# Kernel optimization log

Measured on AMD Instinct MI355X. Metric: run time of the kernel, lower is better.

Reference implementation:

```python
import math
import jax, jax.numpy as jnp
import numpy as np

B, T, C = 2, 2048, 2048
H, G = 16, 4
D = C // H  # head_dim = 128
KV = G * D
SOFT_CAP = 50.0
EPS = 1e-6


def setup_inputs() -> dict:
    key = jax.random.key(0)
    ks = jax.random.split(key, 5)
    s = 1.0 / math.sqrt(C)
    return {
        "x": jax.random.normal(ks[0], (B, T, C), jnp.float32),
        "Wq": jax.random.normal(ks[1], (C, C), jnp.float32) * s,
        "Wk": jax.random.normal(ks[2], (KV, C), jnp.float32) * s,
        "Wv": jax.random.normal(ks[3], (KV, C), jnp.float32) * s,
        "Wo": jax.random.normal(ks[4], (C, C), jnp.float32) * s,
        "bo": jnp.zeros((C,), jnp.float32),
        "q_norm_w": jnp.ones((D,), jnp.float32),
        "k_norm_w": jnp.ones((D,), jnp.float32),
    }


def _rmsnorm(x, w):
    # norm/sqrt(d) formulation, eps added to rms (matches torch module exactly)
    rms = jnp.linalg.norm(x, axis=-1, keepdims=True) / math.sqrt(x.shape[-1])
    return w * (x / (rms + EPS))


def _rotary_tables(seq_len, dim):
    inv_freq = 1.0 / (10000.0 ** (jnp.arange(0, dim, 2, dtype=jnp.float32) / dim))
    t = jnp.arange(seq_len, dtype=jnp.float32)
    freqs = jnp.outer(t, inv_freq)  # [T, D/2]
    return jnp.cos(freqs), jnp.sin(freqs)


def _apply_rope(x, cos, sin):
    # x: [B, T, h, D]; cos/sin: [T, D/2] broadcast as [1, T, 1, D/2]
    d = x.shape[-1] // 2
    x1, x2 = x[..., :d], x[..., d:]
    c = cos[None, :, None, :]
    s = sin[None, :, None, :]
    return jnp.concatenate([x1 * c + x2 * s, -x1 * s + x2 * c], axis=-1)


def reference(x, Wq, Wk, Wv, Wo, bo, q_norm_w, k_norm_w):
    b, t, c = x.shape
    q = (x @ Wq.T).reshape(b, t, H, D)
    k = (x @ Wk.T).reshape(b, t, G, D)
    v = (x @ Wv.T).reshape(b, t, G, D)

    cos, sin = _rotary_tables(t, D)
    q = _apply_rope(_rmsnorm(q, q_norm_w), cos, sin)
    k = _apply_rope(_rmsnorm(k, k_norm_w), cos, sin)

    q = q.transpose(0, 2, 1, 3)              # [B, H, T, D]
    k = jnp.repeat(k.transpose(0, 2, 1, 3), H // G, axis=1)  # [B, H, T, D]
    v = jnp.repeat(v.transpose(0, 2, 1, 3), H // G, axis=1)

    att = jnp.einsum("bhqd,bhkd->bhqk", q, k) / math.sqrt(D)
    causal = jnp.tril(jnp.ones((t, t), bool))
    att = jnp.where(causal[None, None], att, -jnp.inf)
    att = SOFT_CAP * jnp.tanh(att / SOFT_CAP)  # masked entries -> -50
    att = jax.nn.softmax(att, axis=-1)

    y = jnp.einsum("bhqk,bhkd->bhqd", att, v)
    y = y.transpose(0, 2, 1, 3).reshape(b, t, c)
    return y @ Wo.T + bo
```

## Files before the change

kernel.cpp:

```cpp
#include <hip/hip_runtime.h>
#include <math.h>

#define T_SEQ 2048
#define C_DIM 2048
#define NH    16
#define NG    4
#define DH    128
#define BATCH 2

typedef unsigned short u16;
typedef __bf16 bf16_t;
typedef bf16_t bf16x8 __attribute__((ext_vector_type(8)));
typedef float  f32x4  __attribute__((ext_vector_type(4)));

static __device__ __forceinline__ u16 f2bf(float f) {
    return __builtin_bit_cast(u16, (__bf16)f);
}

static __device__ __forceinline__ void gll16(const void* g, void* lds) {
    __builtin_amdgcn_global_load_lds(
        (const __attribute__((address_space(1))) void*)(unsigned long long)(g),
        (__attribute__((address_space(3))) void*)(unsigned int)(unsigned long long)(lds),
        16, 0, 0);
}

__global__ __launch_bounds__(256)
void cast_multi(const float* __restrict__ x,  const float* __restrict__ wq,
                const float* __restrict__ wk, const float* __restrict__ wv,
                u16* __restrict__ xo, u16* __restrict__ wqo,
                u16* __restrict__ wko, u16* __restrict__ wvo) {
    int i = blockIdx.x * 256 + threadIdx.x;
    const float* src; u16* dst; int off;
    if (i < 1048576)      { src = x;  dst = xo;  off = i; }
    else if (i < 1572864) { src = wq; dst = wqo; off = i - 1048576; }
    else if (i < 1703936) { src = wk; dst = wko; off = i - 1572864; }
    else                  { src = wv; dst = wvo; off = i - 1703936; }
    const float4* p = (const float4*)src + (size_t)off * 2;
    float4 a = p[0], b = p[1];
    u16 u[8] = {f2bf(a.x), f2bf(a.y), f2bf(a.z), f2bf(a.w),
                f2bf(b.x), f2bf(b.y), f2bf(b.z), f2bf(b.w)};
    *(uint4*)(dst + (size_t)off * 8) = *(const uint4*)u;
}

__global__ __launch_bounds__(256)
void cast_f32_bf16(const float* __restrict__ in, u16* __restrict__ out, int n8) {
    int i = blockIdx.x * 256 + threadIdx.x;
    if (i >= n8) return;
    const float4* p = (const float4*)in + (size_t)i * 2;
    float4 a = p[0], b = p[1];
    u16 u[8] = {f2bf(a.x), f2bf(a.y), f2bf(a.z), f2bf(a.w),
                f2bf(b.x), f2bf(b.y), f2bf(b.z), f2bf(b.w)};
    *(uint4*)(out + (size_t)i * 8) = *(const uint4*)u;
}

static __device__ __forceinline__ void gemm_body(
        u16* As, u16* Bs,
        const u16* __restrict__ A, const u16* __restrict__ B,
        const float* __restrict__ bias, float* __restrict__ C,
        int N, int K, int m0, int n0) {
    const int t    = threadIdx.x;
    const int lane = t & 63, w = t >> 6;
    const int l15  = lane & 15, quad = lane >> 4;
    const int wr   = w >> 1, wc = w & 1;

    f32x4 acc[4][4];
#pragma unroll
    for (int mt = 0; mt < 4; ++mt)
#pragma unroll
        for (int nt = 0; nt < 4; ++nt) acc[mt][nt] = (f32x4){0.f, 0.f, 0.f, 0.f};

    const int off0 = w*2048 + lane*16;
    const int r0 = off0 >> 6,          c0 = (off0 & 63) >> 1;
    const int r1 = (off0+1024) >> 6,   c1 = ((off0+1024) & 63) >> 1;
    const u16* Ag0 = A + (size_t)(m0 + r0) * K + c0;
    const u16* Ag1 = A + (size_t)(m0 + r1) * K + c1;
    const u16* Bg0 = B + (size_t)(n0 + r0) * K + c0;
    const u16* Bg1 = B + (size_t)(n0 + r1) * K + c1;
    char* AsB = (char*)As; char* BsB = (char*)Bs;
    const int ldsOff0 = w*2048, ldsOff1 = w*2048 + 1024;

    for (int k0 = 0; k0 < K; k0 += 32) {
        gll16(Ag0 + k0, AsB + ldsOff0);
        gll16(Ag1 + k0, AsB + ldsOff1);
        gll16(Bg0 + k0, BsB + ldsOff0);
        gll16(Bg1 + k0, BsB + ldsOff1);
        __syncthreads();
        bf16x8 af[4], bf[4];
#pragma unroll
        for (int mt = 0; mt < 4; ++mt)
            af[mt] = __builtin_bit_cast(bf16x8,
                *(const uint4*)&As[(wr*64 + mt*16 + l15)*32 + quad*8]);
#pragma unroll
        for (int nt = 0; nt < 4; ++nt)
            bf[nt] = __builtin_bit_cast(bf16x8,
                *(const uint4*)&Bs[(wc*64 + nt*16 + l15)*32 + quad*8]);
#pragma unroll
        for (int mt = 0; mt < 4; ++mt)
#pragma unroll
            for (int nt = 0; nt < 4; ++nt)
                acc[mt][nt] = __builtin_amdgcn_mfma_f32_16x16x32_bf16(
                                  af[mt], bf[nt], acc[mt][nt], 0, 0, 0);
        __syncthreads();
    }

#pragma unroll
    for (int mt = 0; mt < 4; ++mt)
#pragma unroll
        for (int nt = 0; nt < 4; ++nt) {
            const int col = n0 + wc*64 + nt*16 + l15;
            const float bv = bias ? bias[col] : 0.f;
#pragma unroll
            for (int r = 0; r < 4; ++r) {
                const int row = m0 + wr*64 + mt*16 + quad*4 + r;
                C[(size_t)row * N + col] = acc[mt][nt][r] + bv;
            }
        }
}

__global__ __launch_bounds__(256)
void gemm_nt_bf16(const u16* __restrict__ A, const u16* __restrict__ B,
                  const float* __restrict__ bias, float* __restrict__ C,
                  int N, int K) {
    __shared__ __align__(16) u16 As[128*32];
    __shared__ __align__(16) u16 Bs[128*32];
    gemm_body(As, Bs, A, B, bias, C, N, K, blockIdx.y*128, blockIdx.x*128);
}

__global__ __launch_bounds__(256)
void gemm_qkv(const u16* __restrict__ A,  const u16* __restrict__ Bq,
              const u16* __restrict__ Bk, const u16* __restrict__ Bv,
              float* __restrict__ Cq, float* __restrict__ Ck, float* __restrict__ Cv) {
    __shared__ __align__(16) u16 As[128*32];
    __shared__ __align__(16) u16 Bs[128*32];
    const int bx = blockIdx.x;
    const u16* B; float* C; int N, n0;
    if (bx < 16)      { B = Bq; C = Cq; N = 2048; n0 = bx * 128; }
    else if (bx < 20) { B = Bk; C = Ck; N = 512;  n0 = (bx-16) * 128; }
    else              { B = Bv; C = Cv; N = 512;  n0 = (bx-20) * 128; }
    gemm_body(As, Bs, A, B, nullptr, C, N, 2048, blockIdx.y*128, n0);
}

__global__ __launch_bounds__(256)
void rmsnorm_rope_qk(const float* __restrict__ qf, const float* __restrict__ kf,
                     const float* __restrict__ qw, const float* __restrict__ kw,
                     u16* __restrict__ qo, u16* __restrict__ ko) {
    const int blk  = blockIdx.x;
    const int sub  = threadIdx.x >> 6;
    const int lane = threadIdx.x & 63;
    const float* in; const float* w; u16* out; int row, nheads; float scale;
    if (blk < 16384) {
        in = qf; w = qw; out = qo; nheads = NH; scale = 0.08838834764831845f;
        row = blk * 4 + sub;
    } else {
        in = kf; w = kw; out = ko; nheads = NG; scale = 1.0f;
        row = (blk - 16384) * 4 + sub;
    }
    const float* p = in + (size_t)row * 128;
    float x1 = p[lane], x2 = p[lane + 64];
    float ss = x1*x1 + x2*x2;
#pragma unroll
    for (int off = 32; off >= 1; off >>= 1) ss += __shfl_xor(ss, off, 64);
    float inv = 1.0f / (sqrtf(ss * (1.0f/128.0f)) + 1e-6f);
    float x1n = w[lane]      * x1 * inv;
    float x2n = w[lane + 64] * x2 * inv;
    int tpos = (row / nheads) & (T_SEQ - 1);
    float invfreq = powf(10000.0f, -(float)lane / 64.0f);
    float s, c;
    sincosf((float)tpos * invfreq, &s, &c);
    out[(size_t)row*128 + lane]      = f2bf((x1n * c + x2n * s) * scale);
    out[(size_t)row*128 + lane + 64] = f2bf((x2n * c - x1n * s) * scale);
}

__global__ __launch_bounds__(256)
void v_cast_transpose(const float* __restrict__ v, u16* __restrict__ vt) {
    __shared__ u16 Lt[128 * 66];
    const int t  = threadIdx.x;
    const int t0 = blockIdx.x * 64;
    const int bg = blockIdx.y;
    const int b  = bg / NG, g = bg % NG;
#pragma unroll
    for (int rep = 0; rep < 8; ++rep) {
        int idx = rep * 256 + t;
        int i   = idx >> 5;
        int c   = idx & 31;
        float4 f = *(const float4*)(v + ((size_t)(b*T_SEQ + t0 + i)*NG + g)*DH + c*4);
        Lt[(c*4+0)*66 + i] = f2bf(f.x);
        Lt[(c*4+1)*66 + i] = f2bf(f.y);
        Lt[(c*4+2)*66 + i] = f2bf(f.z);
        Lt[(c*4+3)*66 + i] = f2bf(f.w);
    }
    __syncthreads();
#pragma unroll
    for (int rep = 0; rep < 4; ++rep) {
        int idx = rep * 256 + t;
        int d = idx >> 3, c = idx & 7;
        const u16* src = &Lt[d*66 + c*8];
        uint4 val;
        val.x = *(const unsigned int*)(src + 0);
        val.y = *(const unsigned int*)(src + 2);
        val.z = *(const unsigned int*)(src + 4);
        val.w = *(const unsigned int*)(src + 6);
        *(uint4*)(vt + ((size_t)(bg*DH + d))*T_SEQ + t0 + c*8) = val;
    }
}

#define KPAD 136
#define VPAD 72
#define PPAD 72

__global__ __launch_bounds__(512)
void flash_attn_mfma(const u16* __restrict__ qh, const u16* __restrict__ kh,
                     const u16* __restrict__ vt, u16* __restrict__ y) {
    __shared__ __align__(16) u16 Ks [64  * KPAD];
    __shared__ __align__(16) u16 Vts[128 * VPAD];
    __shared__ __align__(16) u16 Ps [128 * PPAD];

    const int t    = threadIdx.x;
    const int lane = t & 63, w = t >> 6;
    const int l15  = lane & 15, quad = lane >> 4;
    const int bg   = blockIdx.y;
    const int b    = bg >> 2, g = bg & 3;
    const int chunk = b ? (int)blockIdx.x : (63 - (int)blockIdx.x);
    const int q0   = chunk * 32;
    const int h    = g * (NH / NG) + (w & 3);
    const int qrow0 = q0 + (w >> 2) * 16;

    const float L2E = 1.4426950408889634f;

    bf16x8 aq[4];
    const u16* qp = qh + ((size_t)(b*T_SEQ + qrow0 + l15) * NH + h) * DH;
#pragma unroll
    for (int kc = 0; kc < 4; ++kc)
        aq[kc] = __builtin_bit_cast(bf16x8, *(const uint4*)(qp + kc*32 + quad*8));

    f32x4 accO[8];
#pragma unroll
    for (int nd = 0; nd < 8; ++nd) accO[nd] = (f32x4){0.f, 0.f, 0.f, 0.f};
    float ls[4] = {0.f, 0.f, 0.f, 0.f};

    const int kr = t >> 4, kc16 = t & 15;
    const int vd = t >> 3, vc8  = t & 7;
    const u16* kgb = kh + ((size_t)b*T_SEQ*NG + g)*DH;
    const u16* vgb = vt + ((size_t)(b*NG + g)*DH)*T_SEQ;

    uint4 kreg0, kreg1, vreg0, vreg1;
    {
        kreg0 = *(const uint4*)(kgb + (size_t)(0 + kr)      * NG*DH + kc16*8);
        kreg1 = *(const uint4*)(kgb + (size_t)(0 + kr + 32) * NG*DH + kc16*8);
        vreg0 = *(const uint4*)(vgb + (size_t)vd       * T_SEQ + 0 + vc8*8);
        vreg1 = *(const uint4*)(vgb + (size_t)(vd + 64)* T_SEQ + 0 + vc8*8);
    }

    const int ktiles = q0 / 64 + 1;
    for (int kt = 0; kt < ktiles; ++kt) {
        *(uint4*)&Ks [ kr      *KPAD + kc16*8] = kreg0;
        *(uint4*)&Ks [(kr + 32)*KPAD + kc16*8] = kreg1;
        *(uint4*)&Vts[ vd      *VPAD + vc8*8]  = vreg0;
        *(uint4*)&Vts[(vd + 64)*VPAD + vc8*8]  = vreg1;
        __syncthreads();

        if (kt + 1 < ktiles) {
            const int k1 = (kt + 1) * 64;
            kreg0 = *(const uint4*)(kgb + (size_t)(k1 + kr)      * NG*DH + kc16*8);
            kreg1 = *(const uint4*)(kgb + (size_t)(k1 + kr + 32) * NG*DH + kc16*8);
            vreg0 = *(const uint4*)(vgb + (size_t)vd       * T_SEQ + k1 + vc8*8);
            vreg1 = *(const uint4*)(vgb + (size_t)(vd + 64)* T_SEQ + k1 + vc8*8);
        }

        const int k0 = kt * 64;
        f32x4 accS[4];
#pragma unroll
        for (int nt = 0; nt < 4; ++nt) accS[nt] = (f32x4){0.f, 0.f, 0.f, 0.f};
#pragma unroll
        for (int nt = 0; nt < 4; ++nt)
#pragma unroll
            for (int kc = 0; kc < 4; ++kc) {
                bf16x8 bk = __builtin_bit_cast(bf16x8,
                    *(const uint4*)&Ks[(nt*16 + l15)*KPAD + kc*32 + quad*8]);
                accS[nt] = __builtin_amdgcn_mfma_f32_16x16x32_bf16(aq[kc], bk, accS[nt], 0, 0, 0);
            }

#pragma unroll
        for (int nt = 0; nt < 4; ++nt) {
            const int colg = k0 + nt*16 + l15;
#pragma unroll
            for (int r = 0; r < 4; ++r) {
                const int rowg = qrow0 + quad*4 + r;
                float s = accS[nt][r];
                float z = s * 0.02f;
                float u = z * z;
                float poly = fmaf(u, fmaf(u, fmaf(u, -0.05396825396825397f,
                                       0.13333333333333333f),
                                      -0.3333333333333333f), 1.0f);
                float p = __builtin_amdgcn_exp2f(s * poly * L2E);
                p = (colg > rowg) ? 0.f : p;
                ls[r] += p;
                Ps[(w*16 + quad*4 + r)*PPAD + nt*16 + l15] = f2bf(p);
            }
        }

        bf16x8 ap[2];
#pragma unroll
        for (int kc = 0; kc < 2; ++kc)
            ap[kc] = __builtin_bit_cast(bf16x8,
                *(const uint4*)&Ps[(w*16 + l15)*PPAD + kc*32 + quad*8]);

#pragma unroll
        for (int nd = 0; nd < 8; ++nd)
#pragma unroll
            for (int kc = 0; kc < 2; ++kc) {
                bf16x8 bv = __builtin_bit_cast(bf16x8,
                    *(const uint4*)&Vts[(nd*16 + l15)*VPAD + kc*32 + quad*8]);
                accO[nd] = __builtin_amdgcn_mfma_f32_16x16x32_bf16(ap[kc], bv, accO[nd], 0, 0, 0);
            }
        __syncthreads();
    }

#pragma unroll
    for (int r = 0; r < 4; ++r) {
        float v = ls[r];
        v += __shfl_xor(v, 1, 64);
        v += __shfl_xor(v, 2, 64);
        v += __shfl_xor(v, 4, 64);
        v += __shfl_xor(v, 8, 64);
        ls[r] = v;
    }

#pragma unroll
    for (int r = 0; r < 4; ++r) {
        float invl = 1.f / ls[r];
        u16* yp = y + (size_t)(b*T_SEQ + qrow0 + quad*4 + r) * C_DIM + h*DH;
#pragma unroll
        for (int nd = 0; nd < 8; ++nd)
            yp[nd*16 + l15] = f2bf(accO[nd][r] * invl);
    }
}

extern "C" void kernel_launch(void* const* d_in, const int* in_sizes, int n_in,
                              void* d_out, int out_size, void* d_ws, size_t ws_size,
                              hipStream_t stream) {
    const float* x  = (const float*)d_in[0];
    const float* Wq = (const float*)d_in[1];
    const float* Wk = (const float*)d_in[2];
    const float* Wv = (const float*)d_in[3];
    const float* Wo = (const float*)d_in[4];
    const float* bo = (const float*)d_in[5];
    const float* qw = (const float*)d_in[6];
    const float* kw = (const float*)d_in[7];
    float* out = (float*)d_out;

    const size_t qE = (size_t)BATCH * T_SEQ * NH * DH;
    const size_t kE = (size_t)BATCH * T_SEQ * NG * DH;
    const size_t wqE = (size_t)C_DIM * C_DIM;

    float* qf  = (float*)d_ws;
    float* kf  = qf + qE;
    float* vf  = kf + kE;
    u16*   qh  = (u16*)(vf + kE);
    u16*   khb = qh + qE;
    u16*   vtb = khb + kE;
    u16*   xh  = vtb + kE;
    u16*   wqh = xh + qE;
    u16*   wkh = wqh + wqE;
    u16*   wvh = wkh + (size_t)(NG*DH)*C_DIM;
    u16*   woh = (u16*)kf;
    u16*   yh  = (u16*)qf;

    const int M = BATCH * T_SEQ;
    dim3 blk(256);

    cast_multi<<<dim3(7168), blk, 0, stream>>>(x, Wq, Wk, Wv, xh, wqh, wkh, wvh);

    gemm_qkv<<<dim3(24, M/128), blk, 0, stream>>>(xh, wqh, wkh, wvh, qf, kf, vf);

    rmsnorm_rope_qk<<<dim3(M*NH/4 + M*NG/4), blk, 0, stream>>>(qf, kf, qw, kw, qh, khb);
    v_cast_transpose<<<dim3(T_SEQ/64, BATCH*NG), blk, 0, stream>>>(vf, vtb);

    cast_f32_bf16<<<dim3(wqE/8/256), blk, 0, stream>>>(Wo, woh, wqE/8);

    flash_attn_mfma<<<dim3(T_SEQ/32, BATCH*NG), dim3(512), 0, stream>>>(qh, khb, vtb, yh);

    gemm_nt_bf16<<<dim3(C_DIM/128, M/128), blk, 0, stream>>>(yh, woh, bo, out, C_DIM, C_DIM);
}
```

Measured before the change: 386.7 us.

## Double-buffer K/V via direct-to-LDS loads with swizzle, two query tiles per wave

The flash attention kernel now runs 256 threads. Each wave owns one head and handles two 16-row query tiles, so every K/V fragment read from LDS feeds two MFMAs. K and V tiles are loaded straight into double-buffered LDS with global_load_lds. XOR swizzling replaces row padding to avoid bank conflicts, which removes the register staging and the trailing barrier per tile. The trade-off is more accumulator registers per wave and half as many waves per block, which could reduce latency hiding.

```diff
diff --git a/kernel.cpp b/kernel.cpp
--- a/kernel.cpp
+++ b/kernel.cpp
@@ -204,16 +204,12 @@
     }
 }
 
-#define KPAD 136
-#define VPAD 72
-#define PPAD 72
-
-__global__ __launch_bounds__(512)
+__global__ __launch_bounds__(256, 2)
 void flash_attn_mfma(const u16* __restrict__ qh, const u16* __restrict__ kh,
                      const u16* __restrict__ vt, u16* __restrict__ y) {
-    __shared__ __align__(16) u16 Ks [64  * KPAD];
-    __shared__ __align__(16) u16 Vts[128 * VPAD];
-    __shared__ __align__(16) u16 Ps [128 * PPAD];
+    __shared__ __align__(16) u16 Ks[2][64*128];
+    __shared__ __align__(16) u16 Vs[2][128*64];
+    __shared__ __align__(16) u16 Ps[64*64];
 
     const int t    = threadIdx.x;
     const int lane = t & 63, w = t >> 6;
@@ -222,118 +218,143 @@
     const int b    = bg >> 2, g = bg & 3;
     const int chunk = b ? (int)blockIdx.x : (63 - (int)blockIdx.x);
     const int q0   = chunk * 32;
-    const int h    = g * (NH / NG) + (w & 3);
-    const int qrow0 = q0 + (w >> 2) * 16;
+    const int h    = g * (NH / NG) + w;
 
     const float L2E = 1.4426950408889634f;
 
-    bf16x8 aq[4];
-    const u16* qp = qh + ((size_t)(b*T_SEQ + qrow0 + l15) * NH + h) * DH;
-#pragma unroll
-    for (int kc = 0; kc < 4; ++kc)
-        aq[kc] = __builtin_bit_cast(bf16x8, *(const uint4*)(qp + kc*32 + quad*8));
-
-    f32x4 accO[8];
-#pragma unroll
-    for (int nd = 0; nd < 8; ++nd) accO[nd] = (f32x4){0.f, 0.f, 0.f, 0.f};
-    float ls[4] = {0.f, 0.f, 0.f, 0.f};
-
-    const int kr = t >> 4, kc16 = t & 15;
-    const int vd = t >> 3, vc8  = t & 7;
+    bf16x8 aq[2][4];
+#pragma unroll
+    for (int m = 0; m < 2; ++m) {
+        const u16* qp = qh + ((size_t)(b*T_SEQ + q0 + m*16 + l15) * NH + h) * DH;
+#pragma unroll
+        for (int kc = 0; kc < 4; ++kc)
+            aq[m][kc] = __builtin_bit_cast(bf16x8, *(const uint4*)(qp + kc*32 + quad*8));
+    }
+
+    f32x4 accO[2][8];
+#pragma unroll
+    for (int m = 0; m < 2; ++m)
+#pragma unroll
+        for (int nd = 0; nd < 8; ++nd) accO[m][nd] = (f32x4){0.f, 0.f, 0.f, 0.f};
+    float ls[2][4] = {{0.f,0.f,0.f,0.f},{0.f,0.f,0.f,0.f}};
+
     const u16* kgb = kh + ((size_t)b*T_SEQ*NG + g)*DH;
     const u16* vgb = vt + ((size_t)(b*NG + g)*DH)*T_SEQ;
 
-    uint4 kreg0, kreg1, vreg0, vreg1;
-    {
-        kreg0 = *(const uint4*)(kgb + (size_t)(0 + kr)      * NG*DH + kc16*8);
-        kreg1 = *(const uint4*)(kgb + (size_t)(0 + kr + 32) * NG*DH + kc16*8);
-        vreg0 = *(const uint4*)(vgb + (size_t)vd       * T_SEQ + 0 + vc8*8);
-        vreg1 = *(const uint4*)(vgb + (size_t)(vd + 64)* T_SEQ + 0 + vc8*8);
-    }
-
-    const int ktiles = q0 / 64 + 1;
+    const int krb = t >> 4, kcl = t & 15;
+    const int vdb = t >> 3, vcl = t & 7;
+
+    const int ktiles = q0/64 + 1;
+
+#pragma unroll
+    for (int j = 0; j < 4; ++j) {
+        const int kr = j*16 + krb;
+        gll16(kgb + (size_t)kr*(NG*DH) + ((kcl ^ (kr & 7)) << 3),
+              (char*)Ks[0] + j*4096 + w*1024);
+        const int vd = j*32 + vdb;
+        gll16(vgb + (size_t)vd*T_SEQ + ((vcl ^ (vd & 7)) << 3),
+              (char*)Vs[0] + j*4096 + w*1024);
+    }
+
     for (int kt = 0; kt < ktiles; ++kt) {
-        *(uint4*)&Ks [ kr      *KPAD + kc16*8] = kreg0;
-        *(uint4*)&Ks [(kr + 32)*KPAD + kc16*8] = kreg1;
-        *(uint4*)&Vts[ vd      *VPAD + vc8*8]  = vreg0;
-        *(uint4*)&Vts[(vd + 64)*VPAD + vc8*8]  = vreg1;
+        asm volatile("s_waitcnt vmcnt(0)" ::: "memory");
         __syncthreads();
 
         if (kt + 1 < ktiles) {
-            const int k1 = (kt + 1) * 64;
-            kreg0 = *(const uint4*)(kgb + (size_t)(k1 + kr)      * NG*DH + kc16*8);
-            kreg1 = *(const uint4*)(kgb + (size_t)(k1 + kr + 32) * NG*DH + kc16*8);
-            vreg0 = *(const uint4*)(vgb + (size_t)vd       * T_SEQ + k1 + vc8*8);
-            vreg1 = *(const uint4*)(vgb + (size_t)(vd + 64)* T_SEQ + k1 + vc8*8);
-        }
-
+            const int k0n = (kt + 1) * 64, bn = (kt + 1) & 1;
+#pragma unroll
+            for (int j = 0; j < 4; ++j) {
+                const int kr = j*16 + krb;
+                gll16(kgb + (size_t)(k0n + kr)*(NG*DH) + ((kcl ^ (kr & 7)) << 3),
+                      (char*)Ks[bn] + j*4096 + w*1024);
+                const int vd = j*32 + vdb;
+                gll16(vgb + (size_t)vd*T_SEQ + k0n + ((vcl ^ (vd & 7)) << 3),
+                      (char*)Vs[bn] + j*4096 + w*1024);
+            }
+        }
+
+        const u16* Kb = Ks[kt & 1];
+        const u16* Vb = Vs[kt & 1];
         const int k0 = kt * 64;
-        f32x4 accS[4];
-#pragma unroll
-        for (int nt = 0; nt < 4; ++nt) accS[nt] = (f32x4){0.f, 0.f, 0.f, 0.f};
-#pragma unroll
-        for (int nt = 0; nt < 4; ++nt)
+
+        f32x4 accS[2][4];
+#pragma unroll
+        for (int m = 0; m < 2; ++m)
+#pragma unroll
+            for (int nt = 0; nt < 4; ++nt) accS[m][nt] = (f32x4){0.f,0.f,0.f,0.f};
+
+#pragma unroll
+        for (int nt = 0; nt < 4; ++nt) {
+            const int krow = nt*16 + l15;
+            const int kswz = (krow & 7) << 3;
 #pragma unroll
             for (int kc = 0; kc < 4; ++kc) {
                 bf16x8 bk = __builtin_bit_cast(bf16x8,
-                    *(const uint4*)&Ks[(nt*16 + l15)*KPAD + kc*32 + quad*8]);
-                accS[nt] = __builtin_amdgcn_mfma_f32_16x16x32_bf16(aq[kc], bk, accS[nt], 0, 0, 0);
+                    *(const uint4*)&Kb[krow*128 + ((kc*32 + quad*8) ^ kswz)]);
+                accS[0][nt] = __builtin_amdgcn_mfma_f32_16x16x32_bf16(aq[0][kc], bk, accS[0][nt], 0, 0, 0);
+                accS[1][nt] = __builtin_amdgcn_mfma_f32_16x16x32_bf16(aq[1][kc], bk, accS[1][nt], 0, 0, 0);
             }
-
-#pragma unroll
-        for (int nt = 0; nt < 4; ++nt) {
-            const int colg = k0 + nt*16 + l15;
-#pragma unroll
-            for (int r = 0; r < 4; ++r) {
-                const int rowg = qrow0 + quad*4 + r;
-                float s = accS[nt][r];
-                float z = s * 0.02f;
-                float u = z * z;
-                float poly = fmaf(u, fmaf(u, fmaf(u, -0.05396825396825397f,
-                                       0.13333333333333333f),
-                                      -0.3333333333333333f), 1.0f);
-                float p = __builtin_amdgcn_exp2f(s * poly * L2E);
-                p = (colg > rowg) ? 0.f : p;
-                ls[r] += p;
-                Ps[(w*16 + quad*4 + r)*PPAD + nt*16 + l15] = f2bf(p);
+        }
+
+        bf16x8 ap[2][2];
+#pragma unroll
+        for (int m = 0; m < 2; ++m) {
+#pragma unroll
+            for (int nt = 0; nt < 4; ++nt) {
+                const int colg = k0 + nt*16 + l15;
+#pragma unroll
+                for (int r = 0; r < 4; ++r) {
+                    const int rowg = q0 + m*16 + quad*4 + r;
+                    float s = accS[m][nt][r];
+                    float z = s * 0.02f;
+                    float u = z * z;
+                    float poly = fmaf(u, fmaf(u, fmaf(u, -0.05396825396825397f,
+                                           0.13333333333333333f),
+                                          -0.3333333333333333f), 1.0f);
+                    float p = __builtin_amdgcn_exp2f(s * poly * L2E);
+                    p = (colg > rowg) ? 0.f : p;
+                    ls[m][r] += p;
+                    const int prow = w*16 + quad*4 + r;
+                    Ps[prow*64 + ((nt*16 + l15) ^ ((prow & 7) << 3))] = f2bf(p);
+                }
             }
-        }
-
-        bf16x8 ap[2];
-#pragma unroll
-        for (int kc = 0; kc < 2; ++kc)
-            ap[kc] = __builtin_bit_cast(bf16x8,
-                *(const uint4*)&Ps[(w*16 + l15)*PPAD + kc*32 + quad*8]);
-
-#pragma unroll
-        for (int nd = 0; nd < 8; ++nd)
+            const int arow = w*16 + l15;
+            const int aswz = (arow & 7) << 3;
+            ap[m][0] = __builtin_bit_cast(bf16x8,
+                *(const uint4*)&Ps[arow*64 + ((quad*8)      ^ aswz)]);
+            ap[m][1] = __builtin_bit_cast(bf16x8,
+                *(const uint4*)&Ps[arow*64 + ((32 + quad*8) ^ aswz)]);
+        }
+
+#pragma unroll
+        for (int nd = 0; nd < 8; ++nd) {
+            const int vrow = nd*16 + l15;
+            const int vswz = (vrow & 7) << 3;
 #pragma unroll
             for (int kc = 0; kc < 2; ++kc) {
                 bf16x8 bv = __builtin_bit_cast(bf16x8,
-                    *(const uint4*)&Vts[(nd*16 + l15)*VPAD + kc*32 + quad*8]);
-                accO[nd] = __builtin_amdgcn_mfma_f32_16x16x32_bf16(ap[kc], bv, accO[nd], 0, 0, 0);
+                    *(const uint4*)&Vb[vrow*64 + ((kc*32 + quad*8) ^ vswz)]);
+                accO[0][nd] = __builtin_amdgcn_mfma_f32_16x16x32_bf16(ap[0][kc], bv, accO[0][nd], 0, 0, 0);
+                accO[1][nd] = __builtin_amdgcn_mfma_f32_16x16x32_bf16(ap[1][kc], bv, accO[1][nd], 0, 0, 0);
             }
-        __syncthreads();
-    }
-
-#pragma unroll
-    for (int r = 0; r < 4; ++r) {
-        float v = ls[r];
-        v += __shfl_xor(v, 1, 64);
-        v += __shfl_xor(v, 2, 64);
-        v += __shfl_xor(v, 4, 64);
-        v += __shfl_xor(v, 8, 64);
-        ls[r] = v;
-    }
-
-#pragma unroll
-    for (int r = 0; r < 4; ++r) {
-        float invl = 1.f / ls[r];
-        u16* yp = y + (size_t)(b*T_SEQ + qrow0 + quad*4 + r) * C_DIM + h*DH;
-#pragma unroll
-        for (int nd = 0; nd < 8; ++nd)
-            yp[nd*16 + l15] = f2bf(accO[nd][r] * invl);
-    }
+        }
+    }
+
+#pragma unroll
+    for (int m = 0; m < 2; ++m)
+#pragma unroll
+        for (int r = 0; r < 4; ++r) {
+            float v = ls[m][r];
+            v += __shfl_xor(v, 1, 64);
+            v += __shfl_xor(v, 2, 64);
+            v += __shfl_xor(v, 4, 64);
+            v += __shfl_xor(v, 8, 64);
+            const float invl = 1.f / v;
+            u16* yp = y + (size_t)(b*T_SEQ + q0 + m*16 + quad*4 + r) * C_DIM + h*DH;
+#pragma unroll
+            for (int nd = 0; nd < 8; ++nd)
+                yp[nd*16 + l15] = f2bf(accO[m][nd][r] * invl);
+        }
 }
 
 extern "C" void kernel_launch(void* const* d_in, const int* in_sizes, int n_in,
@@ -378,7 +399,7 @@
 
     cast_f32_bf16<<<dim3(wqE/8/256), blk, 0, stream>>>(Wo, woh, wqE/8);
 
-    flash_attn_mfma<<<dim3(T_SEQ/32, BATCH*NG), dim3(512), 0, stream>>>(qh, khb, vtb, yh);
+    flash_attn_mfma<<<dim3(T_SEQ/32, BATCH*NG), dim3(256), 0, stream>>>(qh, khb, vtb, yh);
 
     gemm_nt_bf16<<<dim3(C_DIM/128, M/128), blk, 0, stream>>>(yh, woh, bo, out, C_DIM, C_DIM);
 }
```

New measurement: 343.2 us. -11.2%, faster.
